# Kernel optimization log

Measured on AMD Instinct MI355X. Metric: run time of the kernel, lower is better.

The kernel has to match this reference:

```python
import jax, jax.numpy as jnp
import numpy as np

HEADS = 8
C_OUT = 256


def _gconv1x1(x, w, g):
    # x: (B, Cin, H, W); w: (Cout, Cin//g) -> grouped 1x1 conv, out (B, g, Cout//g, L)
    B, C, H, W = x.shape
    xr = x.reshape(B, g, C // g, H * W)
    wr = w.reshape(g, w.shape[0] // g, C // g)
    return jnp.einsum('god,bgdl->bgol', wr, xr)


def _sine_pe(d, L, dtype):
    # standard transformer sinusoidal PE laid out as (channels=d, positions=L)
    pos = jnp.arange(L, dtype=jnp.float32)
    i = jnp.arange(0, d, 2, dtype=jnp.float32)
    inv_freq = jnp.exp(-np.float32(np.log(10000.0)) * i / d)  # (d/2,)
    ang = inv_freq[:, None] * pos[None, :]                    # (d/2, L)
    pe = jnp.zeros((d, L), jnp.float32)
    pe = pe.at[0::2].set(jnp.sin(ang)).at[1::2].set(jnp.cos(ang))
    return pe.astype(dtype)


def setup_inputs() -> dict:
    key = jax.random.key(0)
    k1, k2, k3, k4 = jax.random.split(key, 4)
    B, Cin, H, W = 2, 256, 24, 24
    std = np.float32(np.sqrt(2.0 / C_OUT))  # kaiming_normal fan_out, relu gain
    x = jax.random.normal(k1, (B, Cin, H, W), jnp.float32)
    wq = jax.random.normal(k2, (C_OUT, Cin // HEADS), jnp.float32) * std
    wk = jax.random.normal(k3, (C_OUT, Cin // HEADS), jnp.float32) * std
    wv = jax.random.normal(k4, (C_OUT, Cin // HEADS), jnp.float32) * std
    return {"x": x, "wq": wq, "wk": wk, "wv": wv}


def reference(x, wq, wk, wv):
    B, Cin, H, W = x.shape
    g = HEADS
    d = C_OUT // g
    L = H * W
    q = _gconv1x1(x, wq, g)  # (B, g, d, L)
    k = _gconv1x1(x, wk, g)
    v = _gconv1x1(x, wv, g)
    # sinusoidal positional encoding added to keys over flattened spatial dim
    pe = _sine_pe(C_OUT, L, x.dtype)
    k = (k.reshape(B, C_OUT, L) + pe[None]).reshape(B, g, d, L)
    # NOTE: original torch code flattens batch AND heads into the attention dim
    qf = q.transpose(0, 1, 3, 2).reshape(-1, d)   # (N, d), N = B*g*L
    kf = k.transpose(2, 0, 1, 3).reshape(d, -1)   # (d, N)
    vf = v.transpose(0, 1, 3, 2).reshape(-1, d)   # (N, d)
    scale = np.float32(np.sqrt(g / C_OUT))        # = 1/sqrt(d)
    att = jax.nn.softmax(qf @ kf * scale, axis=-1)  # (N, N)
    out = att @ vf                                  # (N, d)
    out = out.reshape(B, g, L, d).transpose(0, 1, 3, 2).reshape(B, C_OUT, H, W)
    return out
```

## Files before the change

kernel.cpp:

```cpp
#include <hip/hip_runtime.h>
#include <hip/hip_bf16.h>


#define LSP   576
#define NROW  9216
#define DH    32
#define NW    16
#define KPW   (NROW / NW)
#define BN    32
#define NTILE (KPW / BN)
#define PSTR  40
#define QB    36
#define SZ    ((size_t)NROW * DH)
#define SZP   (SZ + 4096)

typedef __attribute__((ext_vector_type(8))) short bh8;
typedef __attribute__((ext_vector_type(4))) float f4;

static __device__ __forceinline__ unsigned short f2bf(float x) {
    union { float f; unsigned int i; } w; w.f = x;
    unsigned int u = w.i;
    return (unsigned short)((u + 0x7fffu + ((u >> 16) & 1u)) >> 16);
}
static __device__ __forceinline__ unsigned int pkbf(float a, float b) {
    union { __hip_bfloat162 h2; unsigned int u; } w;
    w.h2 = __float22bfloat162_rn(make_float2(a, b));
    return w.u;
}

#define MFMA(a, b, c) __builtin_amdgcn_mfma_f32_16x16x32_bf16(a, b, c, 0, 0, 0)

__global__ __launch_bounds__(256) void sa_proj_kernel(
    const float* __restrict__ x,
    const float* __restrict__ wq, const float* __restrict__ wk, const float* __restrict__ wv,
    unsigned short* __restrict__ Qhi, unsigned short* __restrict__ Khi,
    unsigned short* __restrict__ Vt)
{
    __shared__ __align__(16) float xs[32 * 40];
    __shared__ float vt[32 * 37];
    __shared__ float wqs[32 * 33], wks[32 * 33], wvs[32 * 33];
    const int t = threadIdx.x;
    const int bg = blockIdx.x >> 4;
    const int part = blockIdx.x & 15;
    const int g = bg & 7;
    const int l0 = part * 36;

    const float* xp = x + (size_t)bg * 32 * LSP + l0;
    for (int i = t; i < 32 * 9; i += 256) {
        int d = i / 9, seg = i % 9;
        *(float4*)(xs + d * 40 + seg * 4) = *(const float4*)(xp + d * LSP + seg * 4);
    }
    for (int i = t; i < 1024; i += 256) {
        int o = i >> 5, d = i & 31;
        wqs[o * 33 + d] = wq[(g * 32 + o) * 32 + d];
        wks[o * 33 + d] = wk[(g * 32 + o) * 32 + d];
        wvs[o * 33 + d] = wv[(g * 32 + o) * 32 + d];
    }
    __syncthreads();

    const float scale = 0.17677669529663687f;
    for (int idx = t; idx < 32 * 36; idx += 256) {
        const int o = idx & 31;
        const int lloc = idx >> 5;
        const int l = l0 + lloc;
        float aq = 0.f, ak = 0.f, av = 0.f;
        #pragma unroll
        for (int d = 0; d < 32; d++) {
            const float xv = xs[d * 40 + lloc];
            aq = fmaf(wqs[o * 33 + d], xv, aq);
            ak = fmaf(wks[o * 33 + d], xv, ak);
            av = fmaf(wvs[o * 33 + d], xv, av);
        }
        aq *= scale;
        const int c = g * 32 + o;
        const float i2 = (float)(c & ~1);
        const float inv = __expf(-0.035977892078031968f * i2);
        float sv, cv;
        __sincosf(inv * (float)l, &sv, &cv);
        ak += (c & 1) ? cv : sv;

        const size_t row = (size_t)bg * LSP + l;
        Qhi[row * 32 + o] = f2bf(aq);
        Khi[row * 32 + o] = f2bf(ak);
        vt[o * 37 + lloc] = av;
    }
    __syncthreads();

    for (int idx = t; idx < 32 * 36; idx += 256) {
        const int d = idx / 36;
        const int cc = idx - d * 36;
        const int n = bg * LSP + l0 + cc;
        const int k = n & 31;
        const int cperm = (k < 16) ? ((k >> 2) * 8 + (k & 3))
                                   : (((k - 16) >> 2) * 8 + ((k - 16) & 3) + 4);
        Vt[(size_t)(n >> 5) * 1024 + d * 32 + cperm] = f2bf(vt[d * 37 + cc]);
    }
}

__global__ __launch_bounds__(1024, 4) void sa_attn_kernel(
    const unsigned short* __restrict__ Qhi, const unsigned short* __restrict__ Khi,
    const unsigned short* __restrict__ Vt, float* __restrict__ out)
{
    __shared__ __align__(16) unsigned short shm[NW * 48 * PSTR];
    const int t = threadIdx.x;
    const int wave = t >> 6, lane = t & 63;
    const int quad = lane >> 4, l16 = lane & 15;
    const int n0 = blockIdx.x * QB;

    unsigned short* psw = shm + wave * 48 * PSTR;

    const bh8 qh0 = *(const bh8*)(Qhi + (size_t)(n0 + l16) * DH + quad * 8);
    const bh8 qh1 = *(const bh8*)(Qhi + (size_t)(n0 + 16 + l16) * DH + quad * 8);
    const bh8 qh2 = *(const bh8*)(Qhi + (size_t)(n0 + 32 + l16) * DH + quad * 8);

    f4 o00 = {0.f,0.f,0.f,0.f}, o01 = {0.f,0.f,0.f,0.f};
    f4 o10 = {0.f,0.f,0.f,0.f}, o11 = {0.f,0.f,0.f,0.f};
    f4 o20 = {0.f,0.f,0.f,0.f}, o21 = {0.f,0.f,0.f,0.f};
    float ls0 = 0.f, ls1 = 0.f, ls2 = 0.f;
    const f4 zf = {0.f,0.f,0.f,0.f};

    const int kbase = wave * KPW;
    const int tile0 = kbase >> 5;

    bh8 kf0 = *(const bh8*)(Khi + (size_t)(kbase + l16) * DH + quad * 8);
    bh8 kf1 = *(const bh8*)(Khi + (size_t)(kbase + 16 + l16) * DH + quad * 8);
    bh8 vf0 = *(const bh8*)(Vt + (size_t)tile0 * 1024 + l16 * 32 + quad * 8);
    bh8 vf1 = *(const bh8*)(Vt + (size_t)tile0 * 1024 + (16 + l16) * 32 + quad * 8);

    for (int tile = 0; tile < NTILE; ++tile) {
        f4 s00 = MFMA(kf0, qh0, zf);
        f4 s01 = MFMA(kf0, qh1, zf);
        f4 s02 = MFMA(kf0, qh2, zf);
        f4 s10 = MFMA(kf1, qh0, zf);
        f4 s11 = MFMA(kf1, qh1, zf);
        f4 s12 = MFMA(kf1, qh2, zf);

        const int tn = (tile + 1 < NTILE) ? tile + 1 : tile;
        const int kn = kbase + tn * BN;
        kf0 = *(const bh8*)(Khi + (size_t)(kn + l16) * DH + quad * 8);
        kf1 = *(const bh8*)(Khi + (size_t)(kn + 16 + l16) * DH + quad * 8);

        uint4 w0, w1, w2;
        {
            float a = __expf(s00[0]), b = __expf(s00[1]),
                  c = __expf(s00[2]), d = __expf(s00[3]);
            ls0 += (a + b) + (c + d);
            w0.x = pkbf(a, b); w0.y = pkbf(c, d);
            a = __expf(s10[0]); b = __expf(s10[1]);
            c = __expf(s10[2]); d = __expf(s10[3]);
            ls0 += (a + b) + (c + d);
            w0.z = pkbf(a, b); w0.w = pkbf(c, d);
        }
        *(uint4*)(psw + l16 * PSTR + quad * 8) = w0;
        {
            float a = __expf(s01[0]), b = __expf(s01[1]),
                  c = __expf(s01[2]), d = __expf(s01[3]);
            ls1 += (a + b) + (c + d);
            w1.x = pkbf(a, b); w1.y = pkbf(c, d);
            a = __expf(s11[0]); b = __expf(s11[1]);
            c = __expf(s11[2]); d = __expf(s11[3]);
            ls1 += (a + b) + (c + d);
            w1.z = pkbf(a, b); w1.w = pkbf(c, d);
        }
        *(uint4*)(psw + (16 + l16) * PSTR + quad * 8) = w1;
        {
            float a = __expf(s02[0]), b = __expf(s02[1]),
                  c = __expf(s02[2]), d = __expf(s02[3]);
            ls2 += (a + b) + (c + d);
            w2.x = pkbf(a, b); w2.y = pkbf(c, d);
            a = __expf(s12[0]); b = __expf(s12[1]);
            c = __expf(s12[2]); d = __expf(s12[3]);
            ls2 += (a + b) + (c + d);
            w2.z = pkbf(a, b); w2.w = pkbf(c, d);
        }
        *(uint4*)(psw + (32 + l16) * PSTR + quad * 8) = w2;

        const bh8 pa0 = *(const bh8*)(psw + l16 * PSTR + quad * 8);
        const bh8 pa1 = *(const bh8*)(psw + (16 + l16) * PSTR + quad * 8);
        const bh8 pa2 = *(const bh8*)(psw + (32 + l16) * PSTR + quad * 8);
        o00 = MFMA(pa0, vf0, o00); o01 = MFMA(pa0, vf1, o01);
        o10 = MFMA(pa1, vf0, o10); o11 = MFMA(pa1, vf1, o11);
        o20 = MFMA(pa2, vf0, o20); o21 = MFMA(pa2, vf1, o21);

        vf0 = *(const bh8*)(Vt + (size_t)(tile0 + tn) * 1024 + l16 * 32 + quad * 8);
        vf1 = *(const bh8*)(Vt + (size_t)(tile0 + tn) * 1024 + (16 + l16) * 32 + quad * 8);
    }

    ls0 += __shfl_xor(ls0, 16); ls0 += __shfl_xor(ls0, 32);
    ls1 += __shfl_xor(ls1, 16); ls1 += __shfl_xor(ls1, 32);
    ls2 += __shfl_xor(ls2, 16); ls2 += __shfl_xor(ls2, 32);

    __syncthreads();
    float* mo = (float*)shm;
    float* mls = mo + 8 * 1536;
    const int mw = wave & 7;
    float* mp = mo + mw * 1536;
    if (wave < 8) {
        #pragma unroll
        for (int reg = 0; reg < 4; ++reg) {
            const int q0 = quad * 4 + reg;
            mp[l16 * 48 + q0]             = o00[reg];
            mp[(16 + l16) * 48 + q0]      = o01[reg];
            mp[l16 * 48 + 16 + q0]        = o10[reg];
            mp[(16 + l16) * 48 + 16 + q0] = o11[reg];
            mp[l16 * 48 + 32 + q0]        = o20[reg];
            mp[(16 + l16) * 48 + 32 + q0] = o21[reg];
        }
        if (quad == 0) {
            mls[mw * 48 + l16]      = ls0;
            mls[mw * 48 + 16 + l16] = ls1;
            mls[mw * 48 + 32 + l16] = ls2;
        }
    }
    __syncthreads();
    if (wave >= 8) {
        #pragma unroll
        for (int reg = 0; reg < 4; ++reg) {
            const int q0 = quad * 4 + reg;
            mp[l16 * 48 + q0]             += o00[reg];
            mp[(16 + l16) * 48 + q0]      += o01[reg];
            mp[l16 * 48 + 16 + q0]        += o10[reg];
            mp[(16 + l16) * 48 + 16 + q0] += o11[reg];
            mp[l16 * 48 + 32 + q0]        += o20[reg];
            mp[(16 + l16) * 48 + 32 + q0] += o21[reg];
        }
        if (quad == 0) {
            mls[mw * 48 + l16]      += ls0;
            mls[mw * 48 + 16 + l16] += ls1;
            mls[mw * 48 + 32 + l16] += ls2;
        }
    }
    __syncthreads();

    const int bg = n0 / LSP;
    const int l0 = n0 - bg * LSP;
    for (int c = t; c < 32 * QB; c += 1024) {
        const int d = c / QB;
        const int q = c - d * QB;
        float num = 0.f, den = 0.f;
        #pragma unroll
        for (int w2 = 0; w2 < 8; ++w2) {
            num += mo[w2 * 1536 + d * 48 + q];
            den += mls[w2 * 48 + q];
        }
        out[((size_t)(bg * 32 + d)) * LSP + l0 + q] = num / den;
    }
}

extern "C" void kernel_launch(void* const* d_in, const int* in_sizes, int n_in,
                              void* d_out, int out_size, void* d_ws, size_t ws_size,
                              hipStream_t stream) {
    (void)in_sizes; (void)n_in; (void)out_size; (void)ws_size;
    const float* x  = (const float*)d_in[0];
    const float* wq = (const float*)d_in[1];
    const float* wk = (const float*)d_in[2];
    const float* wv = (const float*)d_in[3];

    unsigned short* ws = (unsigned short*)d_ws;
    unsigned short* Qhi = ws;
    unsigned short* Khi = ws + SZP;
    unsigned short* Vt  = ws + 2 * SZP;
    float* out = (float*)d_out;

    sa_proj_kernel<<<256, 256, 0, stream>>>(x, wq, wk, wv, Qhi, Khi, Vt);
    sa_attn_kernel<<<256, 1024, 0, stream>>>(Qhi, Khi, Vt, out);
}
```

Baseline: 93.36 us.

## Unroll attention loop by two tiles and use native exp2 with prescaled Q

```diff
diff --git a/kernel.cpp b/kernel.cpp
--- a/kernel.cpp
+++ b/kernel.cpp
@@ -7,8 +7,7 @@
 #define DH    32
 #define NW    16
 #define KPW   (NROW / NW)
-#define BN    32
-#define NTILE (KPW / BN)
+#define NTILE 9
 #define PSTR  40
 #define QB    36
 #define SZ    ((size_t)NROW * DH)
@@ -26,6 +25,13 @@
     union { __hip_bfloat162 h2; unsigned int u; } w;
     w.h2 = __float22bfloat162_rn(make_float2(a, b));
     return w.u;
+}
+static __device__ __forceinline__ float fexp2(float x) {
+#if __has_builtin(__builtin_amdgcn_exp2f)
+    return __builtin_amdgcn_exp2f(x);
+#else
+    return exp2f(x);
+#endif
 }
 
 #define MFMA(a, b, c) __builtin_amdgcn_mfma_f32_16x16x32_bf16(a, b, c, 0, 0, 0)
@@ -58,7 +64,7 @@
     }
     __syncthreads();
 
-    const float scale = 0.17677669529663687f;
+    const float scale = 0.17677669529663687f * 1.4426950408889634f;
     for (int idx = t; idx < 32 * 36; idx += 256) {
         const int o = idx & 31;
         const int lloc = idx >> 5;
@@ -122,68 +128,121 @@
     const int kbase = wave * KPW;
     const int tile0 = kbase >> 5;
 
-    bh8 kf0 = *(const bh8*)(Khi + (size_t)(kbase + l16) * DH + quad * 8);
-    bh8 kf1 = *(const bh8*)(Khi + (size_t)(kbase + 16 + l16) * DH + quad * 8);
-    bh8 vf0 = *(const bh8*)(Vt + (size_t)tile0 * 1024 + l16 * 32 + quad * 8);
-    bh8 vf1 = *(const bh8*)(Vt + (size_t)tile0 * 1024 + (16 + l16) * 32 + quad * 8);
-
-    for (int tile = 0; tile < NTILE; ++tile) {
-        f4 s00 = MFMA(kf0, qh0, zf);
-        f4 s01 = MFMA(kf0, qh1, zf);
-        f4 s02 = MFMA(kf0, qh2, zf);
-        f4 s10 = MFMA(kf1, qh0, zf);
-        f4 s11 = MFMA(kf1, qh1, zf);
-        f4 s12 = MFMA(kf1, qh2, zf);
-
-        const int tn = (tile + 1 < NTILE) ? tile + 1 : tile;
-        const int kn = kbase + tn * BN;
-        kf0 = *(const bh8*)(Khi + (size_t)(kn + l16) * DH + quad * 8);
-        kf1 = *(const bh8*)(Khi + (size_t)(kn + 16 + l16) * DH + quad * 8);
+    bh8 kfa0 = *(const bh8*)(Khi + (size_t)(kbase + l16) * DH + quad * 8);
+    bh8 kfa1 = *(const bh8*)(Khi + (size_t)(kbase + 16 + l16) * DH + quad * 8);
+    bh8 kfb0 = *(const bh8*)(Khi + (size_t)(kbase + 32 + l16) * DH + quad * 8);
+    bh8 kfb1 = *(const bh8*)(Khi + (size_t)(kbase + 48 + l16) * DH + quad * 8);
+    bh8 vfa0 = *(const bh8*)(Vt + (size_t)tile0 * 1024 + l16 * 32 + quad * 8);
+    bh8 vfa1 = *(const bh8*)(Vt + (size_t)tile0 * 1024 + (16 + l16) * 32 + quad * 8);
+    bh8 vfb0 = *(const bh8*)(Vt + (size_t)(tile0 + 1) * 1024 + l16 * 32 + quad * 8);
+    bh8 vfb1 = *(const bh8*)(Vt + (size_t)(tile0 + 1) * 1024 + (16 + l16) * 32 + quad * 8);
+
+    for (int it = 0; it < NTILE; ++it) {
+        const int tn = (it + 1 < NTILE) ? it + 1 : it;
+        const int kna = kbase + tn * 64;
+
+        f4 s00 = MFMA(kfa0, qh0, zf);
+        f4 s01 = MFMA(kfa0, qh1, zf);
+        f4 s02 = MFMA(kfa0, qh2, zf);
+        f4 s10 = MFMA(kfa1, qh0, zf);
+        f4 s11 = MFMA(kfa1, qh1, zf);
+        f4 s12 = MFMA(kfa1, qh2, zf);
+        kfa0 = *(const bh8*)(Khi + (size_t)(kna + l16) * DH + quad * 8);
+        kfa1 = *(const bh8*)(Khi + (size_t)(kna + 16 + l16) * DH + quad * 8);
 
         uint4 w0, w1, w2;
         {
-            float a = __expf(s00[0]), b = __expf(s00[1]),
-                  c = __expf(s00[2]), d = __expf(s00[3]);
+            float a = fexp2(s00[0]), b = fexp2(s00[1]),
+                  c = fexp2(s00[2]), d = fexp2(s00[3]);
             ls0 += (a + b) + (c + d);
             w0.x = pkbf(a, b); w0.y = pkbf(c, d);
-            a = __expf(s10[0]); b = __expf(s10[1]);
-            c = __expf(s10[2]); d = __expf(s10[3]);
+            a = fexp2(s10[0]); b = fexp2(s10[1]);
+            c = fexp2(s10[2]); d = fexp2(s10[3]);
             ls0 += (a + b) + (c + d);
             w0.z = pkbf(a, b); w0.w = pkbf(c, d);
-        }
-        *(uint4*)(psw + l16 * PSTR + quad * 8) = w0;
-        {
-            float a = __expf(s01[0]), b = __expf(s01[1]),
-                  c = __expf(s01[2]), d = __expf(s01[3]);
+            a = fexp2(s01[0]); b = fexp2(s01[1]);
+            c = fexp2(s01[2]); d = fexp2(s01[3]);
             ls1 += (a + b) + (c + d);
             w1.x = pkbf(a, b); w1.y = pkbf(c, d);
-            a = __expf(s11[0]); b = __expf(s11[1]);
-            c = __expf(s11[2]); d = __expf(s11[3]);
+            a = fexp2(s11[0]); b = fexp2(s11[1]);
+            c = fexp2(s11[2]); d = fexp2(s11[3]);
             ls1 += (a + b) + (c + d);
             w1.z = pkbf(a, b); w1.w = pkbf(c, d);
-        }
-        *(uint4*)(psw + (16 + l16) * PSTR + quad * 8) = w1;
-        {
-            float a = __expf(s02[0]), b = __expf(s02[1]),
-                  c = __expf(s02[2]), d = __expf(s02[3]);
+            a = fexp2(s02[0]); b = fexp2(s02[1]);
+            c = fexp2(s02[2]); d = fexp2(s02[3]);
             ls2 += (a + b) + (c + d);
             w2.x = pkbf(a, b); w2.y = pkbf(c, d);
-            a = __expf(s12[0]); b = __expf(s12[1]);
-            c = __expf(s12[2]); d = __expf(s12[3]);
+            a = fexp2(s12[0]); b = fexp2(s12[1]);
+            c = fexp2(s12[2]); d = fexp2(s12[3]);
             ls2 += (a + b) + (c + d);
             w2.z = pkbf(a, b); w2.w = pkbf(c, d);
         }
+        *(uint4*)(psw + l16 * PSTR + quad * 8) = w0;
+        *(uint4*)(psw + (16 + l16) * PSTR + quad * 8) = w1;
         *(uint4*)(psw + (32 + l16) * PSTR + quad * 8) = w2;
 
-        const bh8 pa0 = *(const bh8*)(psw + l16 * PSTR + quad * 8);
-        const bh8 pa1 = *(const bh8*)(psw + (16 + l16) * PSTR + quad * 8);
-        const bh8 pa2 = *(const bh8*)(psw + (32 + l16) * PSTR + quad * 8);
-        o00 = MFMA(pa0, vf0, o00); o01 = MFMA(pa0, vf1, o01);
-        o10 = MFMA(pa1, vf0, o10); o11 = MFMA(pa1, vf1, o11);
-        o20 = MFMA(pa2, vf0, o20); o21 = MFMA(pa2, vf1, o21);
-
-        vf0 = *(const bh8*)(Vt + (size_t)(tile0 + tn) * 1024 + l16 * 32 + quad * 8);
-        vf1 = *(const bh8*)(Vt + (size_t)(tile0 + tn) * 1024 + (16 + l16) * 32 + quad * 8);
+        f4 b00 = MFMA(kfb0, qh0, zf);
+        f4 b01 = MFMA(kfb0, qh1, zf);
+        f4 b02 = MFMA(kfb0, qh2, zf);
+        f4 b10 = MFMA(kfb1, qh0, zf);
+        f4 b11 = MFMA(kfb1, qh1, zf);
+        f4 b12 = MFMA(kfb1, qh2, zf);
+        kfb0 = *(const bh8*)(Khi + (size_t)(kna + 32 + l16) * DH + quad * 8);
+        kfb1 = *(const bh8*)(Khi + (size_t)(kna + 48 + l16) * DH + quad * 8);
+
+        uint4 u0, u1, u2;
+        {
+            float a = fexp2(b00[0]), b = fexp2(b00[1]),
+                  c = fexp2(b00[2]), d = fexp2(b00[3]);
+            ls0 += (a + b) + (c + d);
+            u0.x = pkbf(a, b); u0.y = pkbf(c, d);
+            a = fexp2(b10[0]); b = fexp2(b10[1]);
+            c = fexp2(b10[2]); d = fexp2(b10[3]);
+            ls0 += (a + b) + (c + d);
+            u0.z = pkbf(a, b); u0.w = pkbf(c, d);
+            a = fexp2(b01[0]); b = fexp2(b01[1]);
+            c = fexp2(b01[2]); d = fexp2(b01[3]);
+            ls1 += (a + b) + (c + d);
+            u1.x = pkbf(a, b); u1.y = pkbf(c, d);
+            a = fexp2(b11[0]); b = fexp2(b11[1]);
+            c = fexp2(b11[2]); d = fexp2(b11[3]);
+            ls1 += (a + b) + (c + d);
+            u1.z = pkbf(a, b); u1.w = pkbf(c, d);
+            a = fexp2(b02[0]); b = fexp2(b02[1]);
+            c = fexp2(b02[2]); d = fexp2(b02[3]);
+            ls2 += (a + b) + (c + d);
+            u2.x = pkbf(a, b); u2.y = pkbf(c, d);
+            a = fexp2(b12[0]); b = fexp2(b12[1]);
+            c = fexp2(b12[2]); d = fexp2(b12[3]);
+            ls2 += (a + b) + (c + d);
+            u2.z = pkbf(a, b); u2.w = pkbf(c, d);
+        }
+
+        {
+            const bh8 pa0 = *(const bh8*)(psw + l16 * PSTR + quad * 8);
+            const bh8 pa1 = *(const bh8*)(psw + (16 + l16) * PSTR + quad * 8);
+            const bh8 pa2 = *(const bh8*)(psw + (32 + l16) * PSTR + quad * 8);
+            o00 = MFMA(pa0, vfa0, o00); o01 = MFMA(pa0, vfa1, o01);
+            o10 = MFMA(pa1, vfa0, o10); o11 = MFMA(pa1, vfa1, o11);
+            o20 = MFMA(pa2, vfa0, o20); o21 = MFMA(pa2, vfa1, o21);
+        }
+        vfa0 = *(const bh8*)(Vt + (size_t)(tile0 + 2 * tn) * 1024 + l16 * 32 + quad * 8);
+        vfa1 = *(const bh8*)(Vt + (size_t)(tile0 + 2 * tn) * 1024 + (16 + l16) * 32 + quad * 8);
+
+        *(uint4*)(psw + l16 * PSTR + quad * 8) = u0;
+        *(uint4*)(psw + (16 + l16) * PSTR + quad * 8) = u1;
+        *(uint4*)(psw + (32 + l16) * PSTR + quad * 8) = u2;
+
+        {
+            const bh8 pb0 = *(const bh8*)(psw + l16 * PSTR + quad * 8);
+            const bh8 pb1 = *(const bh8*)(psw + (16 + l16) * PSTR + quad * 8);
+            const bh8 pb2 = *(const bh8*)(psw + (32 + l16) * PSTR + quad * 8);
+            o00 = MFMA(pb0, vfb0, o00); o01 = MFMA(pb0, vfb1, o01);
+            o10 = MFMA(pb1, vfb0, o10); o11 = MFMA(pb1, vfb1, o11);
+            o20 = MFMA(pb2, vfb0, o20); o21 = MFMA(pb2, vfb1, o21);
+        }
+        vfb0 = *(const bh8*)(Vt + (size_t)(tile0 + 2 * tn + 1) * 1024 + l16 * 32 + quad * 8);
+        vfb1 = *(const bh8*)(Vt + (size_t)(tile0 + 2 * tn + 1) * 1024 + (16 + l16) * 32 + quad * 8);
     }
 
     ls0 += __shfl_xor(ls0, 16); ls0 += __shfl_xor(ls0, 32);
```

New measurement: 90.66 us. 2.9% less time.

## Feed softmax probabilities straight from registers into 16x16x16 MFMAs, skipping LDS

Applied to the files above, without the earlier changes.

```diff
diff --git a/kernel.cpp b/kernel.cpp
--- a/kernel.cpp
+++ b/kernel.cpp
@@ -7,14 +7,13 @@
 #define DH    32
 #define NW    16
 #define KPW   (NROW / NW)
-#define BN    32
-#define NTILE (KPW / BN)
-#define PSTR  40
+#define NST   18
 #define QB    36
 #define SZ    ((size_t)NROW * DH)
 #define SZP   (SZ + 4096)
 
 typedef __attribute__((ext_vector_type(8))) short bh8;
+typedef __attribute__((ext_vector_type(4))) short bh4;
 typedef __attribute__((ext_vector_type(4))) float f4;
 
 static __device__ __forceinline__ unsigned short f2bf(float x) {
@@ -27,8 +26,30 @@
     w.h2 = __float22bfloat162_rn(make_float2(a, b));
     return w.u;
 }
+static __device__ __forceinline__ bh4 pack4(float a, float b, float c, float d) {
+    union { unsigned int u[2]; bh4 v; } w;
+    w.u[0] = pkbf(a, b); w.u[1] = pkbf(c, d);
+    return w.v;
+}
+static __device__ __forceinline__ float fexp2(float x) {
+#if __has_builtin(__builtin_amdgcn_exp2f)
+    return __builtin_amdgcn_exp2f(x);
+#else
+    return exp2f(x);
+#endif
+}
 
 #define MFMA(a, b, c) __builtin_amdgcn_mfma_f32_16x16x32_bf16(a, b, c, 0, 0, 0)
+
+#if __has_builtin(__builtin_amdgcn_mfma_f32_16x16x16bf16_1k)
+#define MFMA16(a, b, c) __builtin_amdgcn_mfma_f32_16x16x16bf16_1k(a, b, c, 0, 0, 0)
+#else
+static __device__ __forceinline__ bh8 pad8(bh4 x) {
+    bh8 r = {x[0], x[1], x[2], x[3], 0, 0, 0, 0};
+    return r;
+}
+#define MFMA16(a, b, c) __builtin_amdgcn_mfma_f32_16x16x32_bf16(pad8(a), pad8(b), c, 0, 0, 0)
+#endif
 
 __global__ __launch_bounds__(256) void sa_proj_kernel(
     const float* __restrict__ x,
@@ -58,7 +79,7 @@
     }
     __syncthreads();
 
-    const float scale = 0.17677669529663687f;
+    const float scale = 0.17677669529663687f * 1.4426950408889634f;
     for (int idx = t; idx < 32 * 36; idx += 256) {
         const int o = idx & 31;
         const int lloc = idx >> 5;
@@ -90,10 +111,7 @@
         const int d = idx / 36;
         const int cc = idx - d * 36;
         const int n = bg * LSP + l0 + cc;
-        const int k = n & 31;
-        const int cperm = (k < 16) ? ((k >> 2) * 8 + (k & 3))
-                                   : (((k - 16) >> 2) * 8 + ((k - 16) & 3) + 4);
-        Vt[(size_t)(n >> 5) * 1024 + d * 32 + cperm] = f2bf(vt[d * 37 + cc]);
+        Vt[(size_t)(n >> 5) * 1024 + d * 32 + (n & 31)] = f2bf(vt[d * 37 + cc]);
     }
 }
 
@@ -101,13 +119,11 @@
     const unsigned short* __restrict__ Qhi, const unsigned short* __restrict__ Khi,
     const unsigned short* __restrict__ Vt, float* __restrict__ out)
 {
-    __shared__ __align__(16) unsigned short shm[NW * 48 * PSTR];
+    __shared__ float shm[8 * 1536 + 8 * 48];
     const int t = threadIdx.x;
     const int wave = t >> 6, lane = t & 63;
     const int quad = lane >> 4, l16 = lane & 15;
     const int n0 = blockIdx.x * QB;
-
-    unsigned short* psw = shm + wave * 48 * PSTR;
 
     const bh8 qh0 = *(const bh8*)(Qhi + (size_t)(n0 + l16) * DH + quad * 8);
     const bh8 qh1 = *(const bh8*)(Qhi + (size_t)(n0 + 16 + l16) * DH + quad * 8);
@@ -120,78 +136,78 @@
     const f4 zf = {0.f,0.f,0.f,0.f};
 
     const int kbase = wave * KPW;
-    const int tile0 = kbase >> 5;
+    const int tb = kbase >> 5;
 
     bh8 kf0 = *(const bh8*)(Khi + (size_t)(kbase + l16) * DH + quad * 8);
     bh8 kf1 = *(const bh8*)(Khi + (size_t)(kbase + 16 + l16) * DH + quad * 8);
-    bh8 vf0 = *(const bh8*)(Vt + (size_t)tile0 * 1024 + l16 * 32 + quad * 8);
-    bh8 vf1 = *(const bh8*)(Vt + (size_t)tile0 * 1024 + (16 + l16) * 32 + quad * 8);
-
-    for (int tile = 0; tile < NTILE; ++tile) {
-        f4 s00 = MFMA(kf0, qh0, zf);
-        f4 s01 = MFMA(kf0, qh1, zf);
-        f4 s02 = MFMA(kf0, qh2, zf);
-        f4 s10 = MFMA(kf1, qh0, zf);
-        f4 s11 = MFMA(kf1, qh1, zf);
-        f4 s12 = MFMA(kf1, qh2, zf);
-
-        const int tn = (tile + 1 < NTILE) ? tile + 1 : tile;
-        const int kn = kbase + tn * BN;
-        kf0 = *(const bh8*)(Khi + (size_t)(kn + l16) * DH + quad * 8);
-        kf1 = *(const bh8*)(Khi + (size_t)(kn + 16 + l16) * DH + quad * 8);
-
-        uint4 w0, w1, w2;
+    const unsigned short* vb = Vt + (size_t)tb * 1024;
+    bh4 vl0 = *(const bh4*)(vb + l16 * 32 + quad * 4);
+    bh4 vh0 = *(const bh4*)(vb + l16 * 32 + 16 + quad * 4);
+    bh4 vl1 = *(const bh4*)(vb + (16 + l16) * 32 + quad * 4);
+    bh4 vh1 = *(const bh4*)(vb + (16 + l16) * 32 + 16 + quad * 4);
+
+    for (int st = 0; st < NST; ++st) {
+        const int ns = (st + 1 < NST) ? st + 1 : st;
+
+        const unsigned short* kp = Khi + (size_t)(kbase + ns * 32) * DH;
+        const bh8 nk0 = *(const bh8*)(kp + (size_t)l16 * DH + quad * 8);
+        const bh8 nk1 = *(const bh8*)(kp + (size_t)(16 + l16) * DH + quad * 8);
+        const unsigned short* nvb = Vt + (size_t)(tb + ns) * 1024;
+        const bh4 nvl0 = *(const bh4*)(nvb + l16 * 32 + quad * 4);
+        const bh4 nvh0 = *(const bh4*)(nvb + l16 * 32 + 16 + quad * 4);
+        const bh4 nvl1 = *(const bh4*)(nvb + (16 + l16) * 32 + quad * 4);
+        const bh4 nvh1 = *(const bh4*)(nvb + (16 + l16) * 32 + 16 + quad * 4);
+
+        const f4 s00 = MFMA(kf0, qh0, zf);
+        const f4 s10 = MFMA(kf1, qh0, zf);
+        const f4 s01 = MFMA(kf0, qh1, zf);
+        const f4 s11 = MFMA(kf1, qh1, zf);
+        const f4 s02 = MFMA(kf0, qh2, zf);
+        const f4 s12 = MFMA(kf1, qh2, zf);
+
         {
-            float a = __expf(s00[0]), b = __expf(s00[1]),
-                  c = __expf(s00[2]), d = __expf(s00[3]);
-            ls0 += (a + b) + (c + d);
-            w0.x = pkbf(a, b); w0.y = pkbf(c, d);
-            a = __expf(s10[0]); b = __expf(s10[1]);
-            c = __expf(s10[2]); d = __expf(s10[3]);
-            ls0 += (a + b) + (c + d);
-            w0.z = pkbf(a, b); w0.w = pkbf(c, d);
-        }
-        *(uint4*)(psw + l16 * PSTR + quad * 8) = w0;
+            const float a = fexp2(s00[0]), b = fexp2(s00[1]),
+                        c = fexp2(s00[2]), d = fexp2(s00[3]);
+            const float e = fexp2(s10[0]), f = fexp2(s10[1]),
+                        g = fexp2(s10[2]), h = fexp2(s10[3]);
+            ls0 += ((a + b) + (c + d)) + ((e + f) + (g + h));
+            const bh4 alo = pack4(a, b, c, d);
+            const bh4 ahi = pack4(e, f, g, h);
+            o00 = MFMA16(alo, vl0, o00); o00 = MFMA16(ahi, vh0, o00);
+            o01 = MFMA16(alo, vl1, o01); o01 = MFMA16(ahi, vh1, o01);
+        }
         {
-            float a = __expf(s01[0]), b = __expf(s01[1]),
-                  c = __expf(s01[2]), d = __expf(s01[3]);
-            ls1 += (a + b) + (c + d);
-            w1.x = pkbf(a, b); w1.y = pkbf(c, d);
-            a = __expf(s11[0]); b = __expf(s11[1]);
-            c = __expf(s11[2]); d = __expf(s11[3]);
-            ls1 += (a + b) + (c + d);
-            w1.z = pkbf(a, b); w1.w = pkbf(c, d);
-        }
-        *(uint4*)(psw + (16 + l16) * PSTR + quad * 8) = w1;
+            const float a = fexp2(s01[0]), b = fexp2(s01[1]),
+                        c = fexp2(s01[2]), d = fexp2(s01[3]);
+            const float e = fexp2(s11[0]), f = fexp2(s11[1]),
+                        g = fexp2(s11[2]), h = fexp2(s11[3]);
+            ls1 += ((a + b) + (c + d)) + ((e + f) + (g + h));
+            const bh4 alo = pack4(a, b, c, d);
+            const bh4 ahi = pack4(e, f, g, h);
+            o10 = MFMA16(alo, vl0, o10); o10 = MFMA16(ahi, vh0, o10);
+            o11 = MFMA16(alo, vl1, o11); o11 = MFMA16(ahi, vh1, o11);
+        }
         {
-            float a = __expf(s02[0]), b = __expf(s02[1]),
-                  c = __expf(s02[2]), d = __expf(s02[3]);
-            ls2 += (a + b) + (c + d);
-            w2.x = pkbf(a, b); w2.y = pkbf(c, d);
-            a = __expf(s12[0]); b = __expf(s12[1]);
-            c = __expf(s12[2]); d = __expf(s12[3]);
-            ls2 += (a + b) + (c + d);
-            w2.z = pkbf(a, b); w2.w = pkbf(c, d);
-        }
-        *(uint4*)(psw + (32 + l16) * PSTR + quad * 8) = w2;
-
-        const bh8 pa0 = *(const bh8*)(psw + l16 * PSTR + quad * 8);
-        const bh8 pa1 = *(const bh8*)(psw + (16 + l16) * PSTR + quad * 8);
-        const bh8 pa2 = *(const bh8*)(psw + (32 + l16) * PSTR + quad * 8);
-        o00 = MFMA(pa0, vf0, o00); o01 = MFMA(pa0, vf1, o01);
-        o10 = MFMA(pa1, vf0, o10); o11 = MFMA(pa1, vf1, o11);
-        o20 = MFMA(pa2, vf0, o20); o21 = MFMA(pa2, vf1, o21);
-
-        vf0 = *(const bh8*)(Vt + (size_t)(tile0 + tn) * 1024 + l16 * 32 + quad * 8);
-        vf1 = *(const bh8*)(Vt + (size_t)(tile0 + tn) * 1024 + (16 + l16) * 32 + quad * 8);
+            const float a = fexp2(s02[0]), b = fexp2(s02[1]),
+                        c = fexp2(s02[2]), d = fexp2(s02[3]);
+            const float e = fexp2(s12[0]), f = fexp2(s12[1]),
+                        g = fexp2(s12[2]), h = fexp2(s12[3]);
+            ls2 += ((a + b) + (c + d)) + ((e + f) + (g + h));
+            const bh4 alo = pack4(a, b, c, d);
+            const bh4 ahi = pack4(e, f, g, h);
+            o20 = MFMA16(alo, vl0, o20); o20 = MFMA16(ahi, vh0, o20);
+            o21 = MFMA16(alo, vl1, o21); o21 = MFMA16(ahi, vh1, o21);
+        }
+
+        kf0 = nk0; kf1 = nk1;
+        vl0 = nvl0; vh0 = nvh0; vl1 = nvl1; vh1 = nvh1;
     }
 
     ls0 += __shfl_xor(ls0, 16); ls0 += __shfl_xor(ls0, 32);
     ls1 += __shfl_xor(ls1, 16); ls1 += __shfl_xor(ls1, 32);
     ls2 += __shfl_xor(ls2, 16); ls2 += __shfl_xor(ls2, 32);
 
-    __syncthreads();
-    float* mo = (float*)shm;
+    float* mo = shm;
     float* mls = mo + 8 * 1536;
     const int mw = wave & 7;
     float* mp = mo + mw * 1536;
```

After: 96.85 us. 3.7% more time.
